# Kernel optimization log

Hardware: AMD Instinct MI355X
Metric: run time of the kernel (lower is better)

## Reference

```python
import jax, jax.numpy as jnp
import numpy as np
import math

NLAT, NLON = 46, 90      # equiangular grid (in_shape == out_shape)
CH = 256                 # channels == kdim == vdim
BATCH = 1

def _cc_weights(n):
    # Clenshaw-Curtis quadrature weights (Waldvogel), nodes cos(k*pi/(n-1)); matches torch-harmonics equiangular grid
    n1 = n - 1
    N = np.arange(1, n1, 2)
    l = len(N)
    m = n1 - l
    v = np.concatenate([2.0 / N / (N - 2), [1.0 / N[-1]], np.zeros(m)])
    v = -v[:-1] - v[-1:0:-1]
    g0 = -np.ones(n1)
    g0[l] += n1
    g0[m] += n1
    g = g0 / (n1 ** 2 - 1 + (n1 % 2))
    w = np.fft.ifft(v + g).real
    return np.concatenate([w, w[:1]])

def _precompute_sparsity():
    # replicates _precompute_neighborhood_sparsity_s2: YZY-rotated north pole indicator within theta_cutoff
    lats = np.linspace(0.0, math.pi, NLAT)               # colatitudes of equiangular grid
    quad = (2.0 * math.pi / NLON) * _cc_weights(NLAT)    # per-latitude quadrature weights
    cutoff = math.pi / (NLAT - 1)                        # default theta_cutoff
    lons = np.linspace(0.0, 2.0 * math.pi, NLON + 1)[:-1]
    rows, cols = [], []
    for t in range(NLAT):
        a = -lats[t]
        beta = lons[None, :]
        gamma = lats[:, None]
        z = -np.cos(beta) * np.sin(a) * np.sin(gamma) + np.cos(a) * np.cos(gamma)
        x = np.cos(a) * np.cos(beta) * np.sin(gamma) + np.cos(gamma) * np.sin(a)
        y = np.sin(beta) * np.sin(gamma)
        nrm = np.sqrt(x * x + y * y + z * z)
        theta = np.arccos(np.clip(z / nrm, -1.0, 1.0))
        ii, jj = np.nonzero(theta <= cutoff)
        rows.append(np.full(ii.shape, t, dtype=np.int64))
        cols.append(ii * NLON + jj)
    row_ids = np.concatenate(rows).astype(np.int32)   # CSR row id per nnz (sorted)
    col_idx = np.concatenate(cols).astype(np.int32)   # flattened input index (at wo=0)
    return row_ids, col_idx, quad.astype(np.float32)

def setup_inputs() -> dict:
    key = jax.random.key(0)
    ks = jax.random.split(key, 9)
    row_ids, col_idx, quad = _precompute_sparsity()
    scale = 0.02  # sane init scale (module uses raw randn; trained weights would be O(this))
    return {
        "qo": jax.random.normal(ks[0], (BATCH, CH, NLAT, NLON), dtype=jnp.float32),
        "ki": jax.random.normal(ks[1], (BATCH, CH, NLAT, NLON), dtype=jnp.float32),
        "vi": jax.random.normal(ks[2], (BATCH, CH, NLAT, NLON), dtype=jnp.float32),
        "q_w": jax.random.normal(ks[3], (CH, CH), dtype=jnp.float32) * scale,
        "k_w": jax.random.normal(ks[4], (CH, CH), dtype=jnp.float32) * scale,
        "v_w": jax.random.normal(ks[5], (CH, CH), dtype=jnp.float32) * scale,
        "q_b": jax.random.normal(ks[6], (CH,), dtype=jnp.float32) * scale,
        "k_b": jax.random.normal(ks[7], (CH,), dtype=jnp.float32) * scale,
        "v_b": jax.random.normal(ks[8], (CH,), dtype=jnp.float32) * scale,
        "quad_w": jnp.asarray(quad),
        "row_ids": jnp.asarray(row_ids),
        "col_idx": jnp.asarray(col_idx),
    }

def reference(qo, ki, vi, q_w, k_w, v_w, q_b, k_b, v_b, quad_w, row_ids, col_idx):
    nlat, nlon = qo.shape[2], qo.shape[3]
    # 1x1 conv projections (F.conv2d with [out,in,1,1] kernels)
    q = jnp.einsum("kc,bchw->bkhw", q_w, qo) + q_b[None, :, None, None]
    k = jnp.einsum("kc,bchw->bkhw", k_w, ki) + k_b[None, :, None, None]
    v = jnp.einsum("vc,bchw->bvhw", v_w, vi) + v_b[None, :, None, None]

    hi = col_idx // nlon                                   # [N] input latitude per nnz
    wi0 = col_idx % nlon                                   # [N] input longitude at wo=0
    wo = jnp.arange(nlon)
    wi = (wi0[:, None] + wo[None, :]) % nlon               # [N, nlon] longitudes rotated by output lon

    kg = k[:, :, hi[:, None], wi]                          # [B, kdim, N, nlon] gathered keys
    qg = q[:, :, row_ids, :]                               # [B, kdim, N, nlon] query of owning output row
    qdotk = jnp.einsum("bcnw,bcnw->nbw", qg, kg)           # [N, B, nlon]

    # quadrature-weighted softmax over each output point's neighborhood (segment = output latitude row)
    seg_max = jax.ops.segment_max(qdotk, row_ids, num_segments=nlat, indices_are_sorted=True)
    seg_max = jax.lax.stop_gradient(seg_max)               # max shift cancels exactly in the ratio
    alpha = jnp.exp(qdotk - seg_max[row_ids]) * quad_w[hi][:, None, None]   # [N, B, nlon]
    denom = jax.ops.segment_sum(alpha, row_ids, num_segments=nlat, indices_are_sorted=True)  # [nlat, B, nlon]

    vg = jnp.transpose(v[:, :, hi[:, None], wi], (2, 0, 1, 3))   # [N, B, vdim, nlon]
    num = jax.ops.segment_sum(alpha[:, :, None, :] * vg, row_ids, num_segments=nlat, indices_are_sorted=True)
    out = num / denom[:, :, None, :]                       # [nlat, B, vdim, nlon]
    return jnp.transpose(out, (1, 2, 0, 3))                # [B, vdim, nlat, nlon]
```

## Files before the change

kernel.cpp:

```cpp
#include <hip/hip_runtime.h>
#include <math.h>

#define NLAT 46
#define NLON 90
#define CH   256
#define HW   (NLAT*NLON)

#define LIGHT_PER_XCD 473
#define SLOTS_PER_XCD (45 + LIGHT_PER_XCD)

__device__ __forceinline__ int lower_bound_i(const int* __restrict__ a, int n, int key){
  int lo = 0, hi = n;
  while (lo < hi){ int mid = (lo + hi) >> 1; if (a[mid] < key) lo = mid + 1; else hi = mid; }
  return lo;
}

__global__ __launch_bounds__(256) void proj_kernel(
    const float* __restrict__ qo, const float* __restrict__ ki, const float* __restrict__ vi,
    const float* __restrict__ qw, const float* __restrict__ kw, const float* __restrict__ vw,
    const float* __restrict__ qb, const float* __restrict__ kb, const float* __restrict__ vb,
    float* __restrict__ qT, float* __restrict__ kT, float* __restrict__ vT)
{
  const float *X, *W, *B; float* O;
  if (blockIdx.z == 0)      { X = qo; W = qw; B = qb; O = qT; }
  else if (blockIdx.z == 1) { X = ki; W = kw; B = kb; O = kT; }
  else                      { X = vi; W = vw; B = vb; O = vT; }

  __shared__ float Xs[16][64];
  __shared__ float Ws[16][68];

  const int tid = threadIdx.x;
  const int tx  = tid & 15;
  const int ty  = tid >> 4;
  const int hw0 = blockIdx.x * 64;
  const int k0  = blockIdx.y * 64;

  float acc[4][4];
  #pragma unroll
  for (int i = 0; i < 4; i++)
    #pragma unroll
    for (int j = 0; j < 4; j++) acc[i][j] = 0.f;

  for (int c0 = 0; c0 < CH; c0 += 16){
    {
      int ih = tid & 63;
      int cb = tid >> 6;
      #pragma unroll
      for (int r = 0; r < 4; r++){
        int cc = cb + r*4;
        int hw = hw0 + ih;
        Xs[cc][ih] = (hw < HW) ? X[(size_t)(c0+cc)*HW + hw] : 0.f;
      }
    }
    {
      #pragma unroll
      for (int r = 0; r < 4; r++){
        int idx = tid + r*256;
        int jk = idx >> 4;
        int cc = idx & 15;
        Ws[cc][jk] = W[(size_t)(k0+jk)*CH + c0 + cc];
      }
    }
    __syncthreads();
    #pragma unroll
    for (int cc = 0; cc < 16; cc++){
      float a[4], b[4];
      #pragma unroll
      for (int i = 0; i < 4; i++) a[i] = Xs[cc][ty*4 + i];
      #pragma unroll
      for (int j = 0; j < 4; j++) b[j] = Ws[cc][tx*4 + j];
      #pragma unroll
      for (int i = 0; i < 4; i++)
        #pragma unroll
        for (int j = 0; j < 4; j++)
          acc[i][j] += a[i] * b[j];
    }
    __syncthreads();
  }

  #pragma unroll
  for (int i = 0; i < 4; i++){
    int hw = hw0 + ty*4 + i;
    if (hw >= HW) continue;
    #pragma unroll
    for (int j = 0; j < 4; j++){
      int k = k0 + tx*4 + j;
      O[(size_t)hw*CH + k] = acc[i][j] + B[k];
    }
  }
}

__global__ __launch_bounds__(256) void attn_kernel(
    const float* __restrict__ qT, const float* __restrict__ kT, const float* __restrict__ vT,
    const float* __restrict__ quad_w, const int* __restrict__ row_ids,
    const int* __restrict__ col_idx, int nnz, float* __restrict__ out)
{
  const int bid  = blockIdx.x;
  const int xcd  = bid & 7;
  const int slot = bid >> 3;

  int t, wo;
  if (slot < 45){
    int hu   = xcd * 45 + slot;
    int hidx = hu / 90;
    t  = (hidx < 2) ? hidx : 42 + hidx;
    wo = hu - hidx * 90;
  } else {
    int lu = xcd * LIGHT_PER_XCD + (slot - 45);
    if (lu >= 42 * NLON) return;
    int li = lu / NLON;
    t  = li + 2;
    wo = lu - li * NLON;
  }

  const int tid  = threadIdx.x;
  const int lane = tid & 63;
  const int wave = tid >> 6;

  const int start = lower_bound_i(row_ids, nnz, t);
  const int end   = lower_bound_i(row_ids, nnz, t + 1);

  const float4* qv = (const float4*)(qT + (size_t)(t * NLON + wo) * CH);
  const float4  qf = qv[lane];

  float denom = 0.f;
  float4 acc = make_float4(0.f, 0.f, 0.f, 0.f);

  int n = start + wave;
  for (; n + 4 < end; n += 8){
    int ciA = col_idx[n];
    int hiA = ciA / NLON;
    int wiA = ciA - hiA*NLON + wo; if (wiA >= NLON) wiA -= NLON;
    size_t offA = ((size_t)hiA*NLON + wiA) * CH;
    int ciB = col_idx[n + 4];
    int hiB = ciB / NLON;
    int wiB = ciB - hiB*NLON + wo; if (wiB >= NLON) wiB -= NLON;
    size_t offB = ((size_t)hiB*NLON + wiB) * CH;

    float4 kfA = ((const float4*)(kT + offA))[lane];
    float4 kfB = ((const float4*)(kT + offB))[lane];
    float sA = qf.x*kfA.x + qf.y*kfA.y + qf.z*kfA.z + qf.w*kfA.w;
    float sB = qf.x*kfB.x + qf.y*kfB.y + qf.z*kfB.z + qf.w*kfB.w;
    #pragma unroll
    for (int o = 32; o >= 1; o >>= 1){
      sA += __shfl_xor(sA, o, 64);
      sB += __shfl_xor(sB, o, 64);
    }
    float eA = __expf(sA) * quad_w[hiA];
    float eB = __expf(sB) * quad_w[hiB];
    float4 vfA = ((const float4*)(vT + offA))[lane];
    float4 vfB = ((const float4*)(vT + offB))[lane];
    denom += eA + eB;
    acc.x += eA*vfA.x + eB*vfB.x;
    acc.y += eA*vfA.y + eB*vfB.y;
    acc.z += eA*vfA.z + eB*vfB.z;
    acc.w += eA*vfA.w + eB*vfB.w;
  }
  if (n < end){
    int ci = col_idx[n];
    int hi = ci / NLON;
    int wi = ci - hi*NLON + wo; if (wi >= NLON) wi -= NLON;
    size_t off = ((size_t)hi*NLON + wi) * CH;
    float4 kf = ((const float4*)(kT + off))[lane];
    float s = qf.x*kf.x + qf.y*kf.y + qf.z*kf.z + qf.w*kf.w;
    #pragma unroll
    for (int o = 32; o >= 1; o >>= 1) s += __shfl_xor(s, o, 64);
    float e = __expf(s) * quad_w[hi];
    float4 vf = ((const float4*)(vT + off))[lane];
    denom += e;
    acc.x += e*vf.x; acc.y += e*vf.y; acc.z += e*vf.z; acc.w += e*vf.w;
  }

  __shared__ float sden[4];
  __shared__ float sacc[4][CH];
  if (lane == 0) sden[wave] = denom;
  sacc[wave][lane*4+0] = acc.x;
  sacc[wave][lane*4+1] = acc.y;
  sacc[wave][lane*4+2] = acc.z;
  sacc[wave][lane*4+3] = acc.w;
  __syncthreads();

  const float den = sden[0] + sden[1] + sden[2] + sden[3];
  const float num = sacc[0][tid] + sacc[1][tid] + sacc[2][tid] + sacc[3][tid];
  out[(size_t)tid * HW + t * NLON + wo] = num / den;
}

extern "C" void kernel_launch(void* const* d_in, const int* in_sizes, int n_in,
                              void* d_out, int out_size, void* d_ws, size_t ws_size,
                              hipStream_t stream)
{
  const float* qo   = (const float*)d_in[0];
  const float* ki   = (const float*)d_in[1];
  const float* vi   = (const float*)d_in[2];
  const float* qw   = (const float*)d_in[3];
  const float* kw   = (const float*)d_in[4];
  const float* vw   = (const float*)d_in[5];
  const float* qb   = (const float*)d_in[6];
  const float* kb   = (const float*)d_in[7];
  const float* vb   = (const float*)d_in[8];
  const float* quad = (const float*)d_in[9];
  const int* row_ids = (const int*)d_in[10];
  const int* col_idx = (const int*)d_in[11];
  const int nnz = in_sizes[10];

  float* ws = (float*)d_ws;
  float* qT = ws;
  float* kT = ws + (size_t)HW*CH;
  float* vT = ws + 2*(size_t)HW*CH;

  dim3 gp((HW + 63)/64, CH/64, 3);
  proj_kernel<<<gp, 256, 0, stream>>>(qo, ki, vi, qw, kw, vw, qb, kb, vb, qT, kT, vT);
  attn_kernel<<<dim3(8 * SLOTS_PER_XCD), 256, 0, stream>>>(qT, kT, vT, quad, row_ids, col_idx, nnz, (float*)d_out);
}
```

Baseline: 136.6 us.

## Switch projections to bf16 MFMA and store Q/K/V in bf16

Adds kernels that cast the weights to bf16 and transpose and cast the inputs to channel-last bf16. The projection GEMM is rewritten to use 16x16x32 bf16 MFMA instructions, and the projected Q/K/V are stored as bf16, which halves the gather traffic in the attention kernel. This aims to cut projection compute time and attention memory bandwidth, at the cost of two extra launches and bf16 rounding error in the scores and values.

```diff
diff --git a/kernel.cpp b/kernel.cpp
--- a/kernel.cpp
+++ b/kernel.cpp
@@ -5,9 +5,22 @@
 #define NLON 90
 #define CH   256
 #define HW   (NLAT*NLON)
+#define HWP  4160
 
 #define LIGHT_PER_XCD 473
 #define SLOTS_PER_XCD (45 + LIGHT_PER_XCD)
+
+typedef __attribute__((ext_vector_type(8))) short short8;
+typedef __attribute__((ext_vector_type(4))) float floatx4;
+
+__device__ __forceinline__ ushort f2bf(float f){
+  uint u = __float_as_uint(f);
+  u += 0x7fff + ((u >> 16) & 1);
+  return (ushort)(u >> 16);
+}
+__device__ __forceinline__ float bf2f(ushort u){
+  return __uint_as_float(((uint)u) << 16);
+}
 
 __device__ __forceinline__ int lower_bound_i(const int* __restrict__ a, int n, int key){
   int lo = 0, hi = n;
@@ -15,83 +28,133 @@
   return lo;
 }
 
+__global__ __launch_bounds__(256) void cast_w_kernel(
+    const float* __restrict__ qw, const float* __restrict__ kw, const float* __restrict__ vw,
+    ushort* __restrict__ Wq, ushort* __restrict__ Wk, ushort* __restrict__ Wv)
+{
+  const float* W; ushort* O;
+  if (blockIdx.x == 0){ W = qw; O = Wq; }
+  else if (blockIdx.x == 1){ W = kw; O = Wk; }
+  else { W = vw; O = Wv; }
+  for (int i = threadIdx.x; i < (CH*CH)/4; i += 256){
+    float4 w = ((const float4*)W)[i];
+    ushort4 o;
+    o.x = f2bf(w.x); o.y = f2bf(w.y); o.z = f2bf(w.z); o.w = f2bf(w.w);
+    ((ushort4*)O)[i] = o;
+  }
+}
+
+__global__ __launch_bounds__(256) void transpose_cast_kernel(
+    const float* __restrict__ qo, const float* __restrict__ ki, const float* __restrict__ vi,
+    ushort* __restrict__ qX, ushort* __restrict__ kX, ushort* __restrict__ vX)
+{
+  const float* X; ushort* O;
+  if (blockIdx.z == 0){ X = qo; O = qX; }
+  else if (blockIdx.z == 1){ X = ki; O = kX; }
+  else { X = vi; O = vX; }
+
+  __shared__ float T[64][65];
+
+  const int tid = threadIdx.x;
+  const int hw0 = blockIdx.x * 64;
+  const int c0  = blockIdx.y * 64;
+
+  {
+    int hwL = tid & 63;
+    int cb  = tid >> 6;
+    int hw  = hw0 + hwL;
+    #pragma unroll
+    for (int it = 0; it < 16; it++){
+      int cL = cb + it*4;
+      T[cL][hwL] = (hw < HW) ? X[(size_t)(c0+cL)*HW + hw] : 0.f;
+    }
+  }
+  __syncthreads();
+  {
+    int cpair = tid & 31;
+    int rb    = tid >> 5;
+    #pragma unroll
+    for (int it = 0; it < 8; it++){
+      int r = rb + it*8;
+      float v0 = T[2*cpair][r];
+      float v1 = T[2*cpair+1][r];
+      ushort2 o; o.x = f2bf(v0); o.y = f2bf(v1);
+      *(ushort2*)(O + (size_t)(hw0 + r)*CH + c0 + 2*cpair) = o;
+    }
+  }
+}
+
 __global__ __launch_bounds__(256) void proj_kernel(
-    const float* __restrict__ qo, const float* __restrict__ ki, const float* __restrict__ vi,
-    const float* __restrict__ qw, const float* __restrict__ kw, const float* __restrict__ vw,
+    const ushort* __restrict__ qX, const ushort* __restrict__ kX, const ushort* __restrict__ vX,
+    const ushort* __restrict__ Wq, const ushort* __restrict__ Wk, const ushort* __restrict__ Wv,
     const float* __restrict__ qb, const float* __restrict__ kb, const float* __restrict__ vb,
-    float* __restrict__ qT, float* __restrict__ kT, float* __restrict__ vT)
-{
-  const float *X, *W, *B; float* O;
-  if (blockIdx.z == 0)      { X = qo; W = qw; B = qb; O = qT; }
-  else if (blockIdx.z == 1) { X = ki; W = kw; B = kb; O = kT; }
-  else                      { X = vi; W = vw; B = vb; O = vT; }
-
-  __shared__ float Xs[16][64];
-  __shared__ float Ws[16][68];
-
-  const int tid = threadIdx.x;
-  const int tx  = tid & 15;
-  const int ty  = tid >> 4;
-  const int hw0 = blockIdx.x * 64;
-  const int k0  = blockIdx.y * 64;
-
-  float acc[4][4];
+    ushort* __restrict__ qP, ushort* __restrict__ kP, ushort* __restrict__ vP)
+{
+  const ushort *Xt, *Wb; const float* Bias; ushort* Out;
+  if (blockIdx.z == 0){ Xt = qX; Wb = Wq; Bias = qb; Out = qP; }
+  else if (blockIdx.z == 1){ Xt = kX; Wb = Wk; Bias = kb; Out = kP; }
+  else { Xt = vX; Wb = Wv; Bias = vb; Out = vP; }
+
+  const int tid  = threadIdx.x;
+  const int lane = tid & 63;
+  const int wave = tid >> 6;
+  const int hw_w   = blockIdx.x * 64 + (wave >> 1) * 32;
+  const int kout_w = blockIdx.y * 64 + (wave & 1) * 32;
+
+  const int lm = lane & 15;
+  const int lq = lane >> 4;
+
+  const ushort* a0p = Wb + (size_t)(kout_w + lm)*CH + lq*8;
+  const ushort* a1p = a0p + 16*CH;
+  const ushort* b0p = Xt + (size_t)(hw_w + lm)*CH + lq*8;
+  const ushort* b1p = b0p + 16*CH;
+
+  floatx4 acc00 = {0,0,0,0}, acc01 = {0,0,0,0}, acc10 = {0,0,0,0}, acc11 = {0,0,0,0};
+
   #pragma unroll
-  for (int i = 0; i < 4; i++)
-    #pragma unroll
-    for (int j = 0; j < 4; j++) acc[i][j] = 0.f;
-
-  for (int c0 = 0; c0 < CH; c0 += 16){
-    {
-      int ih = tid & 63;
-      int cb = tid >> 6;
-      #pragma unroll
-      for (int r = 0; r < 4; r++){
-        int cc = cb + r*4;
-        int hw = hw0 + ih;
-        Xs[cc][ih] = (hw < HW) ? X[(size_t)(c0+cc)*HW + hw] : 0.f;
+  for (int k0 = 0; k0 < 8; k0++){
+    int off = k0 * 32;
+    short8 a0 = *(const short8*)(a0p + off);
+    short8 a1 = *(const short8*)(a1p + off);
+    short8 b0 = *(const short8*)(b0p + off);
+    short8 b1 = *(const short8*)(b1p + off);
+    acc00 = __builtin_amdgcn_mfma_f32_16x16x32_bf16(a0, b0, acc00, 0, 0, 0);
+    acc01 = __builtin_amdgcn_mfma_f32_16x16x32_bf16(a0, b1, acc01, 0, 0, 0);
+    acc10 = __builtin_amdgcn_mfma_f32_16x16x32_bf16(a1, b0, acc10, 0, 0, 0);
+    acc11 = __builtin_amdgcn_mfma_f32_16x16x32_bf16(a1, b1, acc11, 0, 0, 0);
+  }
+
+  #pragma unroll
+  for (int i = 0; i < 2; i++){
+    int kout = kout_w + i*16 + lq*4;
+    float4 bias = *(const float4*)(Bias + kout);
+    #pragma unroll
+    for (int j = 0; j < 2; j++){
+      floatx4 c;
+      if (i == 0) c = (j == 0) ? acc00 : acc01;
+      else        c = (j == 0) ? acc10 : acc11;
+      int hw = hw_w + j*16 + lm;
+      if (hw < HW){
+        ushort4 o;
+        o.x = f2bf(c[0] + bias.x);
+        o.y = f2bf(c[1] + bias.y);
+        o.z = f2bf(c[2] + bias.z);
+        o.w = f2bf(c[3] + bias.w);
+        *(ushort4*)(Out + (size_t)hw*CH + kout) = o;
       }
     }
-    {
-      #pragma unroll
-      for (int r = 0; r < 4; r++){
-        int idx = tid + r*256;
-        int jk = idx >> 4;
-        int cc = idx & 15;
-        Ws[cc][jk] = W[(size_t)(k0+jk)*CH + c0 + cc];
-      }
-    }
-    __syncthreads();
-    #pragma unroll
-    for (int cc = 0; cc < 16; cc++){
-      float a[4], b[4];
-      #pragma unroll
-      for (int i = 0; i < 4; i++) a[i] = Xs[cc][ty*4 + i];
-      #pragma unroll
-      for (int j = 0; j < 4; j++) b[j] = Ws[cc][tx*4 + j];
-      #pragma unroll
-      for (int i = 0; i < 4; i++)
-        #pragma unroll
-        for (int j = 0; j < 4; j++)
-          acc[i][j] += a[i] * b[j];
-    }
-    __syncthreads();
-  }
-
-  #pragma unroll
-  for (int i = 0; i < 4; i++){
-    int hw = hw0 + ty*4 + i;
-    if (hw >= HW) continue;
-    #pragma unroll
-    for (int j = 0; j < 4; j++){
-      int k = k0 + tx*4 + j;
-      O[(size_t)hw*CH + k] = acc[i][j] + B[k];
-    }
-  }
+  }
+}
+
+__device__ __forceinline__ float4 ld_bf4(const ushort* p, int lane){
+  ushort4 u = ((const ushort4*)p)[lane];
+  float4 f;
+  f.x = bf2f(u.x); f.y = bf2f(u.y); f.z = bf2f(u.z); f.w = bf2f(u.w);
+  return f;
 }
 
 __global__ __launch_bounds__(256) void attn_kernel(
-    const float* __restrict__ qT, const float* __restrict__ kT, const float* __restrict__ vT,
+    const ushort* __restrict__ qP, const ushort* __restrict__ kP, const ushort* __restrict__ vP,
     const float* __restrict__ quad_w, const int* __restrict__ row_ids,
     const int* __restrict__ col_idx, int nnz, float* __restrict__ out)
 {
@@ -120,8 +183,7 @@
   const int start = lower_bound_i(row_ids, nnz, t);
   const int end   = lower_bound_i(row_ids, nnz, t + 1);
 
-  const float4* qv = (const float4*)(qT + (size_t)(t * NLON + wo) * CH);
-  const float4  qf = qv[lane];
+  const float4 qf = ld_bf4(qP + (size_t)(t * NLON + wo) * CH, lane);
 
   float denom = 0.f;
   float4 acc = make_float4(0.f, 0.f, 0.f, 0.f);
@@ -137,8 +199,8 @@
     int wiB = ciB - hiB*NLON + wo; if (wiB >= NLON) wiB -= NLON;
     size_t offB = ((size_t)hiB*NLON + wiB) * CH;
 
-    float4 kfA = ((const float4*)(kT + offA))[lane];
-    float4 kfB = ((const float4*)(kT + offB))[lane];
+    float4 kfA = ld_bf4(kP + offA, lane);
+    float4 kfB = ld_bf4(kP + offB, lane);
     float sA = qf.x*kfA.x + qf.y*kfA.y + qf.z*kfA.z + qf.w*kfA.w;
     float sB = qf.x*kfB.x + qf.y*kfB.y + qf.z*kfB.z + qf.w*kfB.w;
     #pragma unroll
@@ -148,8 +210,8 @@
     }
     float eA = __expf(sA) * quad_w[hiA];
     float eB = __expf(sB) * quad_w[hiB];
-    float4 vfA = ((const float4*)(vT + offA))[lane];
-    float4 vfB = ((const float4*)(vT + offB))[lane];
+    float4 vfA = ld_bf4(vP + offA, lane);
+    float4 vfB = ld_bf4(vP + offB, lane);
     denom += eA + eB;
     acc.x += eA*vfA.x + eB*vfB.x;
     acc.y += eA*vfA.y + eB*vfB.y;
@@ -161,12 +223,12 @@
     int hi = ci / NLON;
     int wi = ci - hi*NLON + wo; if (wi >= NLON) wi -= NLON;
     size_t off = ((size_t)hi*NLON + wi) * CH;
-    float4 kf = ((const float4*)(kT + off))[lane];
+    float4 kf = ld_bf4(kP + off, lane);
     float s = qf.x*kf.x + qf.y*kf.y + qf.z*kf.z + qf.w*kf.w;
     #pragma unroll
     for (int o = 32; o >= 1; o >>= 1) s += __shfl_xor(s, o, 64);
     float e = __expf(s) * quad_w[hi];
-    float4 vf = ((const float4*)(vT + off))[lane];
+    float4 vf = ld_bf4(vP + off, lane);
     denom += e;
     acc.x += e*vf.x; acc.y += e*vf.y; acc.z += e*vf.z; acc.w += e*vf.w;
   }
@@ -203,12 +265,14 @@
   const int* col_idx = (const int*)d_in[11];
   const int nnz = in_sizes[10];
 
-  float* ws = (float*)d_ws;
-  float* qT = ws;
-  float* kT = ws + (size_t)HW*CH;
-  float* vT = ws + 2*(size_t)HW*CH;
-
-  dim3 gp((HW + 63)/64, CH/64, 3);
-  proj_kernel<<<gp, 256, 0, stream>>>(qo, ki, vi, qw, kw, vw, qb, kb, vb, qT, kT, vT);
-  attn_kernel<<<dim3(8 * SLOTS_PER_XCD), 256, 0, stream>>>(qT, kT, vT, quad, row_ids, col_idx, nnz, (float*)d_out);
-}
+  ushort* ws = (ushort*)d_ws;
+  const size_t TSZ = (size_t)HWP * CH;
+  ushort* qX = ws;              ushort* kX = qX + TSZ;  ushort* vX = kX + TSZ;
+  ushort* qP = vX + TSZ;        ushort* kP = qP + TSZ;  ushort* vP = kP + TSZ;
+  ushort* Wq = vP + TSZ;        ushort* Wk = Wq + CH*CH; ushort* Wv = Wk + CH*CH;
+
+  cast_w_kernel<<<dim3(3), 256, 0, stream>>>(qw, kw, vw, Wq, Wk, Wv);
+  transpose_cast_kernel<<<dim3(65, 4, 3), 256, 0, stream>>>(qo, ki, vi, qX, kX, vX);
+  proj_kernel<<<dim3(65, 4, 3), 256, 0, stream>>>(qX, kX, vX, Wq, Wk, Wv, qb, kb, vb, qP, kP, vP);
+  attn_kernel<<<dim3(8 * SLOTS_PER_XCD), 256, 0, stream>>>(qP, kP, vP, quad, row_ids, col_idx, nnz, (float*)d_out);
+}
```

After: 141.9 us. +3.9%, slower.
